# Optimization experiments

Hardware: AMD Instinct MI355X
Metric: run time of the kernel (lower is better)

## Reference

```python
import jax, jax.numpy as jnp
import numpy as np

B, H, N, D = 8, 12, 1024, 64
SCALE = 1.0 / float(np.sqrt(D))  # 0.125; torch forward default is 1.0 but 1/sqrt(d) is the production value
EPS = 1e-06


def setup_inputs() -> dict:
    key = jax.random.key(0)
    kq, kk, kv = jax.random.split(key, 3)
    q = jax.random.normal(kq, (B, H, N, D), dtype=jnp.float32)
    k = jax.random.normal(kk, (B, H, N, D), dtype=jnp.float32)
    v = jax.random.normal(kv, (B, H, N, D), dtype=jnp.float32)
    # Parameter init per L2Q.__init__: alpha=0.125, beta=0.5, gamma=1/n_tokens
    alpha = jnp.full((H, 1, 1), 0.125, dtype=jnp.float32)
    beta = jnp.full((H, 1, 1), 0.5, dtype=jnp.float32)
    gamma = jnp.full((H, 1, 1), 1.0 / N, dtype=jnp.float32)
    return {"q": q, "k": k, "v": v, "alpha": alpha, "beta": beta, "gamma": gamma}


def reference(q, k, v, alpha, beta, gamma):
    # logits: (B, H, N, N)
    logits = jnp.einsum("bhnd,bhmd->bhnm", q, k) * SCALE
    # per-head quadratic polynomial, then ReLU; params (H,1,1) broadcast over (B,H,N,N)
    attn = jax.nn.relu(alpha * logits * logits + beta * logits + gamma)
    attn = attn / (jnp.sum(attn, axis=-1, keepdims=True) + EPS)
    return jnp.einsum("bhnm,bhmd->bhnd", attn, v)
```

## Files before the change

kernel.cpp:

```cpp
#include <hip/hip_runtime.h>
#include <hip/hip_bf16.h>

typedef __attribute__((ext_vector_type(8))) short bf16x8;
typedef __attribute__((ext_vector_type(4))) float f32x4;
typedef __attribute__((ext_vector_type(16))) float f32x16;

#define MFMA16(a, b, c) __builtin_amdgcn_mfma_f32_16x16x32_bf16(a, b, c, 0, 0, 0)
#define MFMA32(a, b, c) __builtin_amdgcn_mfma_f32_32x32x16_bf16(a, b, c, 0, 0, 0)

static constexpr int kH = 12;
static constexpr int kN = 1024;
static constexpr int kD = 64;
static constexpr int kBH = 96;
static constexpr int kND = kN * kD;
static constexpr float kScale = 0.125f;
static constexpr float kEps = 1e-6f;
static constexpr long kTensorElems = (long)kBH * kND;
static constexpr long kWsNeeded = 2 * kTensorElems * 2;

__device__ __forceinline__ unsigned bfbits(float x) {
    union { __hip_bfloat16 h; unsigned short u; } c;
    c.h = __float2bfloat16(x);
    return (unsigned)c.u;
}
__device__ __forceinline__ unsigned pack2_rne(float a, float b) {
    return bfbits(a) | (bfbits(b) << 16);
}
__device__ __forceinline__ unsigned pack2_rhu(float lo, float hi) {
    unsigned a = __builtin_bit_cast(unsigned, lo) + 0x8000u;
    unsigned b = __builtin_bit_cast(unsigned, hi) + 0x8000u;
    return __builtin_amdgcn_perm(b, a, 0x07060302u);
}

__global__ __launch_bounds__(256, 2) void prep(
    const float* __restrict__ k, const float* __restrict__ v,
    unsigned* __restrict__ klin, unsigned* __restrict__ vlin)
{
    static constexpr int TS = 68;
    __shared__ float T32[64 * TS];
    const int bid = blockIdx.x;
    const int bh = bid >> 4, nt = bid & 15;
    const int t = threadIdx.x;

    const float* kp = k + (long)bh * kND + (long)nt * 64 * kD;
#pragma unroll
    for (int r = 0; r < 4; ++r) {
        const int f4 = t + 256 * r;
        const int n = f4 >> 4, d4 = f4 & 15;
        *(float4*)&T32[n * TS + 4 * d4] = *(const float4*)(kp + (long)n * kD + 4 * d4);
    }
    __syncthreads();
    {
        const int f = t >> 5, sub = t & 31;
        const int s = f >> 1, kb = f & 1;
        unsigned* kdst = klin + (long)bh * (kND / 2) + (long)nt * 2048 + f * 256 + sub * 8;
        uint4 o0, o1;
#pragma unroll
        for (int e = 0; e < 2; ++e) {
            const int l = sub * 2 + e;
            const int hh = l >> 5, l31 = l & 31;
            const float* srcf = &T32[(kb * 32 + l31) * TS + (s * 2 + hh) * 8];
            uint4 o;
            o.x = pack2_rne(srcf[0], srcf[1]);
            o.y = pack2_rne(srcf[2], srcf[3]);
            o.z = pack2_rne(srcf[4], srcf[5]);
            o.w = pack2_rne(srcf[6], srcf[7]);
            if (e == 0) o0 = o; else o1 = o;
        }
        *(uint4*)(kdst)     = o0;
        *(uint4*)(kdst + 4) = o1;
    }
    __syncthreads();

    const float* vp = v + (long)bh * kND + (long)nt * 64 * kD;
#pragma unroll
    for (int r = 0; r < 4; ++r) {
        const int f4 = t + 256 * r;
        const int n = f4 >> 4, d4 = f4 & 15;
        *(float4*)&T32[n * TS + 4 * d4] = *(const float4*)(vp + (long)n * kD + 4 * d4);
    }
    __syncthreads();
    {
        const int d = t >> 2, c = t & 3;
        unsigned u[8];
#pragma unroll
        for (int j = 0; j < 8; ++j) {
            const int key = c * 16 + 2 * j;
            u[j] = pack2_rne(T32[key * TS + d], T32[(key + 1) * TS + d]);
        }
        uint4 A, B;
        A.x = u[0]; A.y = u[1]; A.z = u[4]; A.w = u[5];
        B.x = u[2]; B.y = u[3]; B.z = u[6]; B.w = u[7];
        unsigned* vbase = vlin + (long)bh * (kND / 2);
        const long o0 = (long)nt * 2048 + ((d >> 5) * 4 + c) * 256 + (d & 31) * 4;
        *(uint4*)(vbase + o0)       = A;
        *(uint4*)(vbase + o0 + 128) = B;
    }
}

__global__ __launch_bounds__(256, 3) void l2q_main(
    const float* __restrict__ q,
    const unsigned short* __restrict__ kbf, const unsigned short* __restrict__ vtbf,
    const float* __restrict__ alpha, const float* __restrict__ beta, const float* __restrict__ gamma,
    float* __restrict__ out)
{
    const int bid  = blockIdx.x;
    const int xcd  = bid & 7;
    const int sIdx = bid >> 3;
    const int bh   = xcd * 12 + (sIdx % 12);
    const int qt   = sIdx / 12;
    const int h    = bh % kH;
    const int t    = threadIdx.x;
    const int wave = t >> 6;
    const int lane = t & 63;
    const int l31  = lane & 31;
    const int hh   = lane >> 5;

    const float al = alpha[h] * (kScale * kScale);
    const float be = beta[h] * kScale;
    const float ga = gamma[h];

    const float* qp = q + (long)bh * kND;
    const unsigned* klin = (const unsigned*)kbf + (long)bh * (kND / 2);
    const unsigned* vlin = (const unsigned*)vtbf + (long)bh * (kND / 2);
    const int lane4 = (hh * 32 + l31) * 4;

    bf16x8 qbF[4];
    {
        const int qrow = qt * 128 + wave * 32 + l31;
        const float* qsrc = qp + (long)qrow * kD;
#pragma unroll
        for (int s = 0; s < 4; ++s) {
            const float4 f0 = *(const float4*)(qsrc + s * 16 + hh * 8);
            const float4 f1 = *(const float4*)(qsrc + s * 16 + hh * 8 + 4);
            uint4 u;
            u.x = pack2_rne(f0.x, f0.y);
            u.y = pack2_rne(f0.z, f0.w);
            u.z = pack2_rne(f1.x, f1.y);
            u.w = pack2_rne(f1.z, f1.w);
            qbF[s] = __builtin_bit_cast(bf16x8, u);
        }
    }

    f32x16 oacc[2];
#pragma unroll
    for (int db = 0; db < 2; ++db)
#pragma unroll
        for (int r = 0; r < 16; ++r)
            oacc[db][r] = 0.f;
    float dacc[4] = {0.f, 0.f, 0.f, 0.f};

    for (int tile = 0; tile < 16; ++tile) {
        const unsigned* kt0 = klin + (long)tile * 2048 + lane4;
        const unsigned* vt0 = vlin + (long)tile * 2048 + lane4;
        bf16x8 kfr[8];
        bf16x8 vfr[8];
#pragma unroll
        for (int f = 0; f < 8; ++f)
            kfr[f] = *(const bf16x8*)(kt0 + f * 256);
#pragma unroll
        for (int f = 0; f < 8; ++f)
            vfr[f] = *(const bf16x8*)(vt0 + f * 256);

        f32x16 st[2];
#pragma unroll
        for (int kb = 0; kb < 2; ++kb)
#pragma unroll
            for (int r = 0; r < 16; ++r)
                st[kb][r] = 0.f;
#pragma unroll
        for (int s = 0; s < 4; ++s)
#pragma unroll
            for (int kb = 0; kb < 2; ++kb)
                st[kb] = MFMA32(kfr[s * 2 + kb], qbF[s], st[kb]);

        unsigned u[2][8];
#pragma unroll
        for (int kb = 0; kb < 2; ++kb) {
#pragma unroll
            for (int p = 0; p < 8; ++p) {
                const float s0 = st[kb][2 * p], s1 = st[kb][2 * p + 1];
                const float w0 = fmaxf(fmaf(fmaf(al, s0, be), s0, ga), 0.f);
                const float w1 = fmaxf(fmaf(fmaf(al, s1, be), s1, ga), 0.f);
                dacc[p & 3] += w0 + w1;
                u[kb][p] = pack2_rhu(w0, w1);
            }
        }

#pragma unroll
        for (int s = 0; s < 4; ++s) {
            uint4 fr;
            const int kb = s >> 1, b = (s & 1) * 4;
            fr.x = u[kb][b + 0];
            fr.y = u[kb][b + 1];
            fr.z = u[kb][b + 2];
            fr.w = u[kb][b + 3];
            const bf16x8 pa = __builtin_bit_cast(bf16x8, fr);
            oacc[0] = MFMA32(pa, vfr[s], oacc[0]);
            oacc[1] = MFMA32(pa, vfr[4 + s], oacc[1]);
        }
    }

    float d = (dacc[0] + dacc[1]) + (dacc[2] + dacc[3]);
    d += __shfl_xor(d, 32);
    const float inv = 1.0f / (d + kEps);

    const long obase = (long)bh * kND;
    const int rowbase = qt * 128 + wave * 32;
#pragma unroll
    for (int r = 0; r < 16; ++r) {
        const int row32 = (r & 3) + 8 * (r >> 2) + 4 * hh;
        const float iv = __shfl(inv, row32);
        float* o = out + obase + (long)(rowbase + row32) * kD + l31;
        o[0]  = oacc[0][r] * iv;
        o[32] = oacc[1][r] * iv;
    }
}

static constexpr int KSU = 36;
static constexpr int VSU = 36;
static constexpr int PSU = 36;

__global__ __launch_bounds__(256, 3) void l2q_attn_fb(
    const float* __restrict__ q, const float* __restrict__ k, const float* __restrict__ v,
    const float* __restrict__ alpha, const float* __restrict__ beta, const float* __restrict__ gamma,
    float* __restrict__ out)
{
    __shared__ __align__(16) unsigned KsU[64 * KSU];
    __shared__ __align__(16) unsigned VtU[64 * VSU];
    __shared__ __align__(16) unsigned PU[128 * PSU];

    const int bid  = blockIdx.x;
    const int bh   = bid >> 3;
    const int qt   = bid & 7;
    const int h    = bh % kH;
    const int t    = threadIdx.x;
    const int wave = t >> 6;
    const int lane = t & 63;
    const int quad = lane >> 4;
    const int l15  = lane & 15;

    const float al = alpha[h], be = beta[h], ga = gamma[h];

    const long base = (long)bh * kN * kD;
    const float* qp = q + base;
    const float* kp = k + base;
    const float* vp = v + base;

    bf16x8 qa[2][2];
#pragma unroll
    for (int rb = 0; rb < 2; ++rb) {
        const int row = qt * 128 + wave * 32 + rb * 16 + l15;
#pragma unroll
        for (int kc = 0; kc < 2; ++kc) {
            const float* src = qp + (long)row * kD + kc * 32 + quad * 8;
            const float4 f0 = *(const float4*)(src);
            const float4 f1 = *(const float4*)(src + 4);
            uint4 u;
            u.x = pack2_rne(f0.x, f0.y);
            u.y = pack2_rne(f0.z, f0.w);
            u.z = pack2_rne(f1.x, f1.y);
            u.w = pack2_rne(f1.z, f1.w);
            qa[rb][kc] = __builtin_bit_cast(bf16x8, u);
        }
    }

    f32x4 oacc[2][4];
#pragma unroll
    for (int rb = 0; rb < 2; ++rb)
#pragma unroll
        for (int db = 0; db < 4; ++db)
            oacc[rb][db] = (f32x4){0.f, 0.f, 0.f, 0.f};

    float dsum[2][4] = {{0.f, 0.f, 0.f, 0.f}, {0.f, 0.f, 0.f, 0.f}};
    unsigned* Pw = &PU[wave * 32 * PSU];

    for (int tile = 0; tile < 16; ++tile) {
        __syncthreads();
        const int k0 = tile * 64;
#pragma unroll
        for (int r = 0; r < 4; ++r) {
            const int f4 = t + 256 * r;
            const int n = f4 >> 4, d4 = f4 & 15;
            const float4 kg = *(const float4*)(kp + (long)(k0 + n) * kD + 4 * d4);
            uint2 pk;
            pk.x = pack2_rne(kg.x, kg.y);
            pk.y = pack2_rne(kg.z, kg.w);
            *(uint2*)&KsU[n * KSU + 2 * d4] = pk;
        }
#pragma unroll
        for (int r = 0; r < 2; ++r) {
            const int u = t + 256 * r;
            const int key2 = u & 31, d4 = u >> 5;
            const float* s0 = vp + (long)(k0 + 2 * key2) * kD + 4 * d4;
            const float4 va = *(const float4*)(s0);
            const float4 vb = *(const float4*)(s0 + kD);
            VtU[(4 * d4 + 0) * VSU + key2] = pack2_rne(va.x, vb.x);
            VtU[(4 * d4 + 1) * VSU + key2] = pack2_rne(va.y, vb.y);
            VtU[(4 * d4 + 2) * VSU + key2] = pack2_rne(va.z, vb.z);
            VtU[(4 * d4 + 3) * VSU + key2] = pack2_rne(va.w, vb.w);
        }
        __syncthreads();

        f32x4 s[2][4];
#pragma unroll
        for (int rb = 0; rb < 2; ++rb)
#pragma unroll
            for (int nb = 0; nb < 4; ++nb)
                s[rb][nb] = (f32x4){0.f, 0.f, 0.f, 0.f};
#pragma unroll
        for (int nb = 0; nb < 4; ++nb) {
            bf16x8 kb0 = *(const bf16x8*)&KsU[(nb * 16 + l15) * KSU + 4 * quad];
            bf16x8 kb1 = *(const bf16x8*)&KsU[(nb * 16 + l15) * KSU + 16 + 4 * quad];
#pragma unroll
            for (int rb = 0; rb < 2; ++rb) {
                s[rb][nb] = MFMA16(qa[rb][0], kb0, s[rb][nb]);
                s[rb][nb] = MFMA16(qa[rb][1], kb1, s[rb][nb]);
            }
        }

        const bool ev = (lane & 1) == 0;
#pragma unroll
        for (int rb = 0; rb < 2; ++rb) {
#pragma unroll
            for (int nb = 0; nb < 4; ++nb) {
                float w0, w1, w2, w3;
                {
                    float l0 = s[rb][nb][0] * kScale;
                    float l1 = s[rb][nb][1] * kScale;
                    float l2 = s[rb][nb][2] * kScale;
                    float l3 = s[rb][nb][3] * kScale;
                    w0 = fmaxf(fmaf(fmaf(al, l0, be), l0, ga), 0.f);
                    w1 = fmaxf(fmaf(fmaf(al, l1, be), l1, ga), 0.f);
                    w2 = fmaxf(fmaf(fmaf(al, l2, be), l2, ga), 0.f);
                    w3 = fmaxf(fmaf(fmaf(al, l3, be), l3, ga), 0.f);
                }
                dsum[rb][0] += w0; dsum[rb][1] += w1;
                dsum[rb][2] += w2; dsum[rb][3] += w3;

                const float o0 = __shfl_xor(w0, 1);
                const float o1 = __shfl_xor(w1, 1);
                const float o2 = __shfl_xor(w2, 1);
                const float o3 = __shfl_xor(w3, 1);
                const unsigned pa = ev ? pack2_rne(w0, o0) : pack2_rne(o2, w2);
                const unsigned pb = ev ? pack2_rne(w1, o1) : pack2_rne(o3, w3);
                const int r0 = ev ? 0 : 2;
                const int cu = (16 * nb + (l15 & ~1)) >> 1;
                const int rowb = rb * 16 + quad * 4 + r0;
                Pw[rowb * PSU + cu] = pa;
                Pw[(rowb + 1) * PSU + cu] = pb;
            }
        }

        bf16x8 pf[2][2];
#pragma unroll
        for (int rb = 0; rb < 2; ++rb)
#pragma unroll
            for (int kc = 0; kc < 2; ++kc)
                pf[rb][kc] = *(const bf16x8*)&Pw[(rb * 16 + l15) * PSU + 16 * kc + 4 * quad];
#pragma unroll
        for (int db = 0; db < 4; ++db) {
            bf16x8 vf0 = *(const bf16x8*)&VtU[(db * 16 + l15) * VSU + 4 * quad];
            bf16x8 vf1 = *(const bf16x8*)&VtU[(db * 16 + l15) * VSU + 16 + 4 * quad];
#pragma unroll
            for (int rb = 0; rb < 2; ++rb) {
                oacc[rb][db] = MFMA16(pf[rb][0], vf0, oacc[rb][db]);
                oacc[rb][db] = MFMA16(pf[rb][1], vf1, oacc[rb][db]);
            }
        }
    }

#pragma unroll
    for (int rb = 0; rb < 2; ++rb)
#pragma unroll
        for (int i = 0; i < 4; ++i) {
            float d = dsum[rb][i];
            d += __shfl_xor(d, 1);
            d += __shfl_xor(d, 2);
            d += __shfl_xor(d, 4);
            d += __shfl_xor(d, 8);
            dsum[rb][i] = 1.0f / (d + kEps);
        }

#pragma unroll
    for (int rb = 0; rb < 2; ++rb)
#pragma unroll
        for (int db = 0; db < 4; ++db)
#pragma unroll
            for (int i = 0; i < 4; ++i) {
                const int row = qt * 128 + wave * 32 + rb * 16 + quad * 4 + i;
                out[base + (long)row * kD + db * 16 + l15] = oacc[rb][db][i] * dsum[rb][i];
            }
}

extern "C" void kernel_launch(void* const* d_in, const int* in_sizes, int n_in,
                              void* d_out, int out_size, void* d_ws, size_t ws_size,
                              hipStream_t stream) {
    const float* q     = (const float*)d_in[0];
    const float* k     = (const float*)d_in[1];
    const float* v     = (const float*)d_in[2];
    const float* alpha = (const float*)d_in[3];
    const float* beta  = (const float*)d_in[4];
    const float* gamma = (const float*)d_in[5];
    float* out = (float*)d_out;

    if (ws_size < (size_t)kWsNeeded) {
        l2q_attn_fb<<<dim3(768), dim3(256), 0, stream>>>(q, k, v, alpha, beta, gamma, out);
        return;
    }

    unsigned* klin = (unsigned*)d_ws;
    unsigned* vlin = klin + kTensorElems / 2;

    prep<<<dim3(1536), dim3(256), 0, stream>>>(k, v, klin, vlin);
    l2q_main<<<dim3(768), dim3(256), 0, stream>>>(
        q, (const unsigned short*)klin, (const unsigned short*)vlin,
        alpha, beta, gamma, out);
}
```

Measured before the change: 146.6 us.

## Split key range across wave pairs and reduce partial outputs via LDS

Each block now covers 64 query rows instead of 128. Two waves share each 32-row strip and each handles half of the key tiles. Partial output accumulators and denominators are combined through shared memory before normalisation. The grid doubles to 1536 blocks and launch bounds go up to 4 blocks per CU, with V fragments loaded in two halves to lower register pressure. The aim is more parallelism and occupancy, at the cost of an LDS reduction, a block barrier and idle waves during the epilogue.

```diff
diff --git a/kernel.cpp b/kernel.cpp
--- a/kernel.cpp
+++ b/kernel.cpp
@@ -98,12 +98,15 @@
     }
 }
 
-__global__ __launch_bounds__(256, 3) void l2q_main(
+__global__ __launch_bounds__(256, 4) void l2q_main(
     const float* __restrict__ q,
     const unsigned short* __restrict__ kbf, const unsigned short* __restrict__ vtbf,
     const float* __restrict__ alpha, const float* __restrict__ beta, const float* __restrict__ gamma,
     float* __restrict__ out)
 {
+    __shared__ float Ob[2][32 * 64];
+    __shared__ float Db[2][32];
+
     const int bid  = blockIdx.x;
     const int xcd  = bid & 7;
     const int sIdx = bid >> 3;
@@ -112,6 +115,8 @@
     const int h    = bh % kH;
     const int t    = threadIdx.x;
     const int wave = t >> 6;
+    const int strip = wave & 1;
+    const int khalf = wave >> 1;
     const int lane = t & 63;
     const int l31  = lane & 31;
     const int hh   = lane >> 5;
@@ -127,7 +132,7 @@
 
     bf16x8 qbF[4];
     {
-        const int qrow = qt * 128 + wave * 32 + l31;
+        const int qrow = qt * 64 + strip * 32 + l31;
         const float* qsrc = qp + (long)qrow * kD;
 #pragma unroll
         for (int s = 0; s < 4; ++s) {
@@ -150,17 +155,15 @@
             oacc[db][r] = 0.f;
     float dacc[4] = {0.f, 0.f, 0.f, 0.f};
 
-    for (int tile = 0; tile < 16; ++tile) {
+    for (int it = 0; it < 8; ++it) {
+        const int tile = khalf * 8 + it;
         const unsigned* kt0 = klin + (long)tile * 2048 + lane4;
         const unsigned* vt0 = vlin + (long)tile * 2048 + lane4;
+
         bf16x8 kfr[8];
-        bf16x8 vfr[8];
 #pragma unroll
         for (int f = 0; f < 8; ++f)
             kfr[f] = *(const bf16x8*)(kt0 + f * 256);
-#pragma unroll
-        for (int f = 0; f < 8; ++f)
-            vfr[f] = *(const bf16x8*)(vt0 + f * 256);
 
         f32x16 st[2];
 #pragma unroll
@@ -173,6 +176,11 @@
 #pragma unroll
             for (int kb = 0; kb < 2; ++kb)
                 st[kb] = MFMA32(kfr[s * 2 + kb], qbF[s], st[kb]);
+
+        bf16x8 vfr0[4];
+#pragma unroll
+        for (int f = 0; f < 4; ++f)
+            vfr0[f] = *(const bf16x8*)(vt0 + f * 256);
 
         unsigned u[2][8];
 #pragma unroll
@@ -195,25 +203,54 @@
             fr.y = u[kb][b + 1];
             fr.z = u[kb][b + 2];
             fr.w = u[kb][b + 3];
-            const bf16x8 pa = __builtin_bit_cast(bf16x8, fr);
-            oacc[0] = MFMA32(pa, vfr[s], oacc[0]);
-            oacc[1] = MFMA32(pa, vfr[4 + s], oacc[1]);
+            oacc[0] = MFMA32(__builtin_bit_cast(bf16x8, fr), vfr0[s], oacc[0]);
+        }
+
+        bf16x8 vfr1[4];
+#pragma unroll
+        for (int f = 0; f < 4; ++f)
+            vfr1[f] = *(const bf16x8*)(vt0 + (4 + f) * 256);
+
+#pragma unroll
+        for (int s = 0; s < 4; ++s) {
+            uint4 fr;
+            const int kb = s >> 1, b = (s & 1) * 4;
+            fr.x = u[kb][b + 0];
+            fr.y = u[kb][b + 1];
+            fr.z = u[kb][b + 2];
+            fr.w = u[kb][b + 3];
+            oacc[1] = MFMA32(__builtin_bit_cast(bf16x8, fr), vfr1[s], oacc[1]);
         }
     }
 
     float d = (dacc[0] + dacc[1]) + (dacc[2] + dacc[3]);
     d += __shfl_xor(d, 32);
-    const float inv = 1.0f / (d + kEps);
-
-    const long obase = (long)bh * kND;
-    const int rowbase = qt * 128 + wave * 32;
-#pragma unroll
-    for (int r = 0; r < 16; ++r) {
-        const int row32 = (r & 3) + 8 * (r >> 2) + 4 * hh;
-        const float iv = __shfl(inv, row32);
-        float* o = out + obase + (long)(rowbase + row32) * kD + l31;
-        o[0]  = oacc[0][r] * iv;
-        o[32] = oacc[1][r] * iv;
+
+    if (khalf == 1) {
+        float* ob = &Ob[strip][0];
+#pragma unroll
+        for (int r = 0; r < 16; ++r) {
+            const int row32 = (r & 3) + 8 * (r >> 2) + 4 * hh;
+            ob[row32 * 64 + l31]      = oacc[0][r];
+            ob[row32 * 64 + 32 + l31] = oacc[1][r];
+        }
+        if (hh == 0) Db[strip][l31] = d;
+    }
+    __syncthreads();
+    if (khalf == 0) {
+        const float dt = d + Db[strip][l31];
+        const float inv = 1.0f / (dt + kEps);
+        const float* ob = &Ob[strip][0];
+        const long obase = (long)bh * kND;
+        const int rowbase = qt * 64 + strip * 32;
+#pragma unroll
+        for (int r = 0; r < 16; ++r) {
+            const int row32 = (r & 3) + 8 * (r >> 2) + 4 * hh;
+            const float iv = __shfl(inv, row32);
+            float* o = out + obase + (long)(rowbase + row32) * kD + l31;
+            o[0]  = (oacc[0][r] + ob[row32 * 64 + l31])      * iv;
+            o[32] = (oacc[1][r] + ob[row32 * 64 + 32 + l31]) * iv;
+        }
     }
 }
 
@@ -413,7 +450,7 @@
     unsigned* vlin = klin + kTensorElems / 2;
 
     prep<<<dim3(1536), dim3(256), 0, stream>>>(k, v, klin, vlin);
-    l2q_main<<<dim3(768), dim3(256), 0, stream>>>(
+    l2q_main<<<dim3(1536), dim3(256), 0, stream>>>(
         q, (const unsigned short*)klin, (const unsigned short*)vlin,
         alpha, beta, gamma, out);
 }
```

After: 171.8 us. +17.2%, slower.
